# Kernel optimization log

Measured on AMD Instinct MI355X. Metric: run time of the kernel, lower is better.

The kernel has to match this reference:

```python
import jax, jax.numpy as jnp
import numpy as np

B, N, TF, DM = 16, 4096, 512, 1024

def next_fast_len(n):
    # smallest 5-smooth number >= n (matches scipy.fftpack.next_fast_len)
    while True:
        m = n
        for p in (2, 3, 5):
            while m % p == 0:
                m //= p
        if m == 1:
            return n
        n += 1

def conv1d_fft(x, weights):
    # x: (..., N, F), weights: (M,); causal exponentially-weighted correlation
    n = x.shape[-2]
    m = weights.shape[-1]
    L = next_fast_len(n + m - 1)
    f_x = jnp.fft.rfft(x, n=L, axis=-2)                 # (..., Lr, F) complex
    f_w = jnp.fft.rfft(weights, n=L, axis=-1)           # (Lr,)
    out = jnp.fft.irfft(f_x * jnp.conj(f_w)[..., None], L, axis=-2)
    out = jnp.roll(out, -1, axis=-2)
    return out[..., L - n:, :]                           # last N along seq axis

def setup_inputs() -> dict:
    key = jax.random.key(0)
    ks = jax.random.split(key, 8)
    inp = {
        "x": jax.random.normal(ks[0], (B, N, TF), dtype=jnp.float32),
        "latent_growth": jax.random.normal(ks[1], (B, N, DM), dtype=jnp.float32),
        "latent_seasonal": jax.random.normal(ks[2], (B, N, DM), dtype=jnp.float32),
        "alpha": jnp.zeros((1,), dtype=jnp.float32),  # nn.Parameter(torch.Tensor([0.0]))
        "w_growth": jax.random.normal(ks[3], (TF, DM), dtype=jnp.float32) / np.sqrt(DM),
        "b_growth": jnp.zeros((TF,), dtype=jnp.float32),
        "w_seasonal": jax.random.normal(ks[4], (TF, DM), dtype=jnp.float32) / np.sqrt(DM),
        "b_seasonal": jnp.zeros((TF,), dtype=jnp.float32),
    }
    return inp

def reference(x, latent_growth, latent_seasonal, alpha, w_growth, b_growth, w_seasonal, b_seasonal):
    n = x.shape[1]
    a = jax.nn.sigmoid(alpha)[0]
    powers = jnp.arange(n, dtype=x.dtype)[::-1]          # flipped arange
    seasonal = jnp.einsum('bnd,fd->bnf', latent_seasonal, w_seasonal) + b_seasonal
    aes_weights = a * (1.0 - a) ** powers                # alpha*(1-alpha)^k EMA kernel
    seasonal_normalized_term = conv1d_fft(x - seasonal, aes_weights)
    # NOTE: the original module computes `growth` but does not use it in the output
    growth = jnp.einsum('bnd,fd->bnf', latent_growth, w_growth) + b_growth
    growth_term = conv1d_fft(x, aes_weights)
    return seasonal_normalized_term + growth_term
```

## Files before the change

### kernel.cpp

```cpp
#include <hip/hip_runtime.h>
#include <math.h>

#define B_DIM 16
#define N_SEQ 4096
#define TF_DIM 512
#define DM_DIM 1024
#define CHUNK 128
#define NCHUNK (N_SEQ / CHUNK)
#define NKT (DM_DIM / 32)

typedef __attribute__((ext_vector_type(4))) float f32x4;
typedef __attribute__((ext_vector_type(8))) short bf16x8;
typedef unsigned short u16;
typedef unsigned int u32;

__device__ __forceinline__ u16 f2bf(float f) {
    u32 u = __builtin_bit_cast(u32, f);
    u += 0x7fffu + ((u >> 16) & 1u);
    return (u16)(u >> 16);
}

__device__ __forceinline__ u32 cvtpk(float lo, float hi) {
    u32 r;
    asm("v_cvt_pk_bf16_f32 %0, %1, %2" : "=v"(r) : "v"(lo), "v"(hi));
    return r;
}

__device__ __forceinline__ void gload16(const u16* g, u16* l) {
    __builtin_amdgcn_global_load_lds(
        (const __attribute__((address_space(1))) void*)g,
        (__attribute__((address_space(3))) void*)l, 16, 0, 0);
}

#define SYNC_DRAIN() asm volatile("s_waitcnt vmcnt(0)\n\ts_barrier" ::: "memory")

__global__ __launch_bounds__(256)
void cvt_bf16(const float* __restrict__ ls, const float* __restrict__ wm,
              u16* __restrict__ lsb, u16* __restrict__ wmb)
{
    const size_t LSG = (size_t)B_DIM * N_SEQ * DM_DIM / 4;
    const size_t i = (size_t)blockIdx.x * 256 + threadIdx.x;
    const float* src;
    u16* dst;
    if (i < LSG) { src = ls + i * 4; dst = lsb + i * 4; }
    else         { const size_t j = i - LSG; src = wm + j * 4; dst = wmb + j * 4; }
    const f32x4 v = *(const f32x4*)src;
    u32* d = (u32*)dst;
    d[0] = cvtpk(v[0], v[1]);
    d[1] = cvtpk(v[2], v[3]);
}

__global__ __launch_bounds__(256, 2)
void gemm_u_kernel(const float* __restrict__ x,
                   const u16* __restrict__ lsb,
                   const u16* __restrict__ wmb,
                   const float* __restrict__ bias,
                   const float* __restrict__ alpha,
                   u16* __restrict__ u,
                   float* __restrict__ e)
{
    __shared__ u16 As[2][4096];
    __shared__ u16 Ws[2][4096];
    __shared__ float red[2][4][16];

    const int tid = threadIdx.x;

    const int s  = blockIdx.x;
    const int kk = s >> 3;
    const int fb = kk & 3;
    const int rp = (s & 7) + ((kk >> 2) << 3);
    const int f0   = fb * 128;
    const int row0 = rp * 128;

    const int lane = tid & 63;
    const int wid  = tid >> 6;
    const int wm = wid >> 1, wn = wid & 1;
    const int l15 = lane & 15, l4 = lane >> 4;

    const int G0 = wid * 128 + lane;
    const int G1 = G0 + 64;
    int row_a, slot_a, row_b, slot_b;
    { const int r = G0 >> 2;
      row_a  = (r & ~1) | ((r ^ (G0 >> 4)) & 1);
      slot_a = (G0 & 3) ^ (row_a & 3); }
    { const int r = G1 >> 2;
      row_b  = (r & ~1) | ((r ^ (G1 >> 4)) & 1);
      slot_b = (G1 & 3) ^ (row_b & 3); }

    const u16* aSrc0 = lsb + (size_t)(row0 + row_a) * DM_DIM + slot_a * 8;
    const u16* aSrc1 = lsb + (size_t)(row0 + row_b) * DM_DIM + slot_b * 8;
    const u16* wSrc0 = wmb + (size_t)(f0 + row_a) * DM_DIM + slot_a * 8;
    const u16* wSrc1 = wmb + (size_t)(f0 + row_b) * DM_DIM + slot_b * 8;

#define STAGE(BUF, KT) do {                                              \
        const int _o = (KT) * 32;                                        \
        gload16(aSrc0 + _o, &As[BUF][wid * 1024]);                       \
        gload16(aSrc1 + _o, &As[BUF][wid * 1024 + 512]);                 \
        gload16(wSrc0 + _o, &Ws[BUF][wid * 1024]);                       \
        gload16(wSrc1 + _o, &Ws[BUF][wid * 1024 + 512]);                 \
    } while (0)

    int rofa[4], rofw[4];
    const int rxor = (l15 & 7) << 3;
#pragma unroll
    for (int i = 0; i < 4; ++i) {
        rofa[i] = ((wm * 64 + i * 16 + l15) * 32 + l4 * 8) ^ rxor;
        rofw[i] = ((wn * 64 + i * 16 + l15) * 32 + l4 * 8) ^ rxor;
    }

    f32x4 acc[4][4];
#pragma unroll
    for (int i = 0; i < 4; ++i)
#pragma unroll
        for (int j = 0; j < 4; ++j) acc[i][j] = (f32x4){0.f, 0.f, 0.f, 0.f};

#define COMPUTE(BUF) do {                                                \
        const u16* _Ab = As[BUF];                                        \
        const u16* _Wb = Ws[BUF];                                        \
        bf16x8 _af[4], _wf[4];                                           \
        _Pragma("unroll")                                                \
        for (int i = 0; i < 4; ++i) {                                    \
            _af[i] = *(const bf16x8*)(_Ab + rofa[i]);                    \
            _wf[i] = *(const bf16x8*)(_Wb + rofw[i]);                    \
        }                                                                \
        _Pragma("unroll")                                                \
        for (int mi = 0; mi < 4; ++mi)                                   \
        _Pragma("unroll")                                                \
        for (int ni = 0; ni < 4; ++ni)                                   \
            acc[mi][ni] = __builtin_amdgcn_mfma_f32_16x16x32_bf16(       \
                _af[mi], _wf[ni], acc[mi][ni], 0, 0, 0);                 \
    } while (0)

    STAGE(0, 0);
    SYNC_DRAIN();

#pragma unroll 1
    for (int kt = 0; kt < NKT; kt += 2) {
        if (kt + 1 < NKT) STAGE(1, kt + 1);
        COMPUTE(0);
        SYNC_DRAIN();

        if (kt + 2 < NKT) STAGE(0, kt + 2);
        COMPUTE(1);
        SYNC_DRAIN();
    }

    const float a = 1.0f / (1.0f + expf(-alpha[0]));
    const float c = 1.0f - a;
    const float l2c = log2f(c);

    float bia[4];
#pragma unroll
    for (int ni = 0; ni < 4; ++ni) bia[ni] = bias[f0 + wn * 64 + ni * 16 + l15];

    float epart[4] = {0.f, 0.f, 0.f, 0.f};

#pragma unroll
    for (int mi = 0; mi < 4; ++mi) {
#pragma unroll
        for (int j = 0; j < 4; ++j) {
            const int r = wm * 64 + mi * 16 + l4 * 4 + j;
            const size_t rb = (size_t)(row0 + r) * TF_DIM;
            const float wgt = (r == CHUNK - 1)
                                  ? a
                                  : a * exp2f((float)(CHUNK - 1 - r) * l2c);
#pragma unroll
            for (int ni = 0; ni < 4; ++ni) {
                const int f = f0 + wn * 64 + ni * 16 + l15;
                const float uval = 2.0f * x[rb + f] - (acc[mi][ni][j] + bia[ni]);
                u[rb + f] = f2bf(uval);
                epart[ni] = fmaf(wgt, uval, epart[ni]);
            }
        }
    }

#pragma unroll
    for (int ni = 0; ni < 4; ++ni) {
        epart[ni] += __shfl_xor(epart[ni], 16, 64);
        epart[ni] += __shfl_xor(epart[ni], 32, 64);
    }
    if (wm == 1 && l4 == 0) {
#pragma unroll
        for (int ni = 0; ni < 4; ++ni) red[wn][ni][l15] = epart[ni];
    }
    __syncthreads();
    if (wm == 0 && l4 == 0) {
#pragma unroll
        for (int ni = 0; ni < 4; ++ni) {
            const int f = f0 + wn * 64 + ni * 16 + l15;
            e[(size_t)rp * TF_DIM + f] = epart[ni] + red[wn][ni][l15];
        }
    }
}

__global__ __launch_bounds__(256)
void ema_carry(const float* __restrict__ e, const float* __restrict__ alpha,
               float* __restrict__ carry)
{
    const int idx = blockIdx.x * 256 + threadIdx.x;
    const int f = idx & (TF_DIM - 1);
    const int b = idx >> 9;
    const float a = 1.0f / (1.0f + expf(-alpha[0]));
    const float c = 1.0f - a;
    const float cC = exp2f((float)CHUNK * log2f(c));
    const size_t base = (size_t)b * NCHUNK * TF_DIM + f;
    float Y = 0.0f;
    carry[base] = 0.0f;
    for (int ch = 1; ch < NCHUNK; ++ch) {
        Y = fmaf(cC, Y, e[base + (size_t)(ch - 1) * TF_DIM]);
        carry[base + (size_t)ch * TF_DIM] = Y;
    }
}

__global__ __launch_bounds__(256)
void ema_apply(const u16* __restrict__ u, const float* __restrict__ carry,
               const float* __restrict__ alpha, float* __restrict__ out)
{
    const int bc = blockIdx.x;
    const int tid = threadIdx.x;
    const float a = 1.0f / (1.0f + expf(-alpha[0]));
    const float c = 1.0f - a;
    float y0 = carry[(size_t)bc * TF_DIM + 2 * tid];
    float y1 = carry[(size_t)bc * TF_DIM + 2 * tid + 1];
    const u32* up = (const u32*)(u + (size_t)bc * CHUNK * TF_DIM) + tid;
    float2*    op = (float2*)(out + (size_t)bc * CHUNK * TF_DIM) + tid;
#pragma unroll 4
    for (int j = 0; j < CHUNK; ++j) {
        const u32 w = up[(size_t)j * (TF_DIM / 2)];
        const float u0 = __builtin_bit_cast(float, (w & 0xffffu) << 16);
        const float u1 = __builtin_bit_cast(float, (w >> 16) << 16);
        y0 = fmaf(c, y0, a * u0);
        y1 = fmaf(c, y1, a * u1);
        op[(size_t)j * (TF_DIM / 2)] = make_float2(y0, y1);
    }
}

extern "C" void kernel_launch(void* const* d_in, const int* in_sizes, int n_in,
                              void* d_out, int out_size, void* d_ws, size_t ws_size,
                              hipStream_t stream) {
    const float* x     = (const float*)d_in[0];
    const float* ls    = (const float*)d_in[2];
    const float* alpha = (const float*)d_in[3];
    const float* wmat  = (const float*)d_in[6];
    const float* bias  = (const float*)d_in[7];
    float* out = (float*)d_out;

    u16*   u     = (u16*)d_ws;
    u16*   lsb   = u + (size_t)B_DIM * N_SEQ * TF_DIM;
    u16*   wmb   = lsb + (size_t)B_DIM * N_SEQ * DM_DIM;
    float* e     = (float*)(wmb + (size_t)TF_DIM * DM_DIM);
    float* carry = e + (size_t)B_DIM * NCHUNK * TF_DIM;

    const int cvt_blocks = (B_DIM * N_SEQ * DM_DIM / 4 + TF_DIM * DM_DIM / 4) / 256;
    cvt_bf16<<<cvt_blocks, 256, 0, stream>>>(ls, wmat, lsb, wmb);

    gemm_u_kernel<<<2048, 256, 0, stream>>>(x, lsb, wmb, bias, alpha, u, e);

    ema_carry<<<(B_DIM * TF_DIM) / 256, 256, 0, stream>>>(e, alpha, carry);
    ema_apply<<<B_DIM * NCHUNK, 256, 0, stream>>>(u, carry, alpha, out);
}
```

Measured before the change: 253.3 us.

## Enlarge GEMM tile to 256x128 with 512-thread blocks and simpler LDS swizzle

After: 244.4 us. -3.5%, faster.

```diff
diff --git a/kernel.cpp b/kernel.cpp
--- a/kernel.cpp
+++ b/kernel.cpp
@@ -50,7 +50,7 @@
     d[1] = cvtpk(v[2], v[3]);
 }
 
-__global__ __launch_bounds__(256, 2)
+__global__ __launch_bounds__(512, 4)
 void gemm_u_kernel(const float* __restrict__ x,
                    const u16* __restrict__ lsb,
                    const u16* __restrict__ wmb,
@@ -59,9 +59,9 @@
                    u16* __restrict__ u,
                    float* __restrict__ e)
 {
-    __shared__ u16 As[2][4096];
+    __shared__ u16 As[2][8192];
     __shared__ u16 Ws[2][4096];
-    __shared__ float red[2][4][16];
+    __shared__ float red[2][2][4][16];
 
     const int tid = threadIdx.x;
 
@@ -70,42 +70,32 @@
     const int fb = kk & 3;
     const int rp = (s & 7) + ((kk >> 2) << 3);
     const int f0   = fb * 128;
-    const int row0 = rp * 128;
+    const int row0 = rp * 256;
 
     const int lane = tid & 63;
     const int wid  = tid >> 6;
     const int wm = wid >> 1, wn = wid & 1;
     const int l15 = lane & 15, l4 = lane >> 4;
 
-    const int G0 = wid * 128 + lane;
-    const int G1 = G0 + 64;
-    int row_a, slot_a, row_b, slot_b;
-    { const int r = G0 >> 2;
-      row_a  = (r & ~1) | ((r ^ (G0 >> 4)) & 1);
-      slot_a = (G0 & 3) ^ (row_a & 3); }
-    { const int r = G1 >> 2;
-      row_b  = (r & ~1) | ((r ^ (G1 >> 4)) & 1);
-      slot_b = (G1 & 3) ^ (row_b & 3); }
-
-    const u16* aSrc0 = lsb + (size_t)(row0 + row_a) * DM_DIM + slot_a * 8;
-    const u16* aSrc1 = lsb + (size_t)(row0 + row_b) * DM_DIM + slot_b * 8;
-    const u16* wSrc0 = wmb + (size_t)(f0 + row_a) * DM_DIM + slot_a * 8;
-    const u16* wSrc1 = wmb + (size_t)(f0 + row_b) * DM_DIM + slot_b * 8;
+    const int srow = lane >> 2;
+    const int sgc  = (lane & 3) ^ (srow & 3);
+    const u16* pA = lsb + (size_t)(row0 + wid * 32 + srow) * DM_DIM + sgc * 8;
+    const u16* pW = wmb + (size_t)(f0 + wid * 16 + srow) * DM_DIM + sgc * 8;
 
 #define STAGE(BUF, KT) do {                                              \
         const int _o = (KT) * 32;                                        \
-        gload16(aSrc0 + _o, &As[BUF][wid * 1024]);                       \
-        gload16(aSrc1 + _o, &As[BUF][wid * 1024 + 512]);                 \
-        gload16(wSrc0 + _o, &Ws[BUF][wid * 1024]);                       \
-        gload16(wSrc1 + _o, &Ws[BUF][wid * 1024 + 512]);                 \
+        gload16(pA + _o,                 &As[BUF][wid * 1024]);          \
+        gload16(pA + _o + 16 * DM_DIM,   &As[BUF][wid * 1024 + 512]);    \
+        gload16(pW + _o,                 &Ws[BUF][wid * 512]);           \
     } while (0)
 
     int rofa[4], rofw[4];
-    const int rxor = (l15 & 7) << 3;
 #pragma unroll
     for (int i = 0; i < 4; ++i) {
-        rofa[i] = ((wm * 64 + i * 16 + l15) * 32 + l4 * 8) ^ rxor;
-        rofw[i] = ((wn * 64 + i * 16 + l15) * 32 + l4 * 8) ^ rxor;
+        const int ra = wm * 64 + i * 16 + l15;
+        const int rw = wn * 64 + i * 16 + l15;
+        rofa[i] = ra * 32 + ((l4 ^ (ra & 3)) * 8);
+        rofw[i] = rw * 32 + ((l4 ^ (rw & 3)) * 8);
     }
 
     f32x4 acc[4][4];
@@ -160,10 +150,11 @@
 #pragma unroll
         for (int j = 0; j < 4; ++j) {
             const int r = wm * 64 + mi * 16 + l4 * 4 + j;
+            const int rc = r & (CHUNK - 1);
             const size_t rb = (size_t)(row0 + r) * TF_DIM;
-            const float wgt = (r == CHUNK - 1)
+            const float wgt = (rc == CHUNK - 1)
                                   ? a
-                                  : a * exp2f((float)(CHUNK - 1 - r) * l2c);
+                                  : a * exp2f((float)(CHUNK - 1 - rc) * l2c);
 #pragma unroll
             for (int ni = 0; ni < 4; ++ni) {
                 const int f = f0 + wn * 64 + ni * 16 + l15;
@@ -179,16 +170,17 @@
         epart[ni] += __shfl_xor(epart[ni], 16, 64);
         epart[ni] += __shfl_xor(epart[ni], 32, 64);
     }
-    if (wm == 1 && l4 == 0) {
-#pragma unroll
-        for (int ni = 0; ni < 4; ++ni) red[wn][ni][l15] = epart[ni];
+    const int ch = wm >> 1;
+    if ((wm & 1) == 1 && l4 == 0) {
+#pragma unroll
+        for (int ni = 0; ni < 4; ++ni) red[ch][wn][ni][l15] = epart[ni];
     }
     __syncthreads();
-    if (wm == 0 && l4 == 0) {
+    if ((wm & 1) == 0 && l4 == 0) {
 #pragma unroll
         for (int ni = 0; ni < 4; ++ni) {
             const int f = f0 + wn * 64 + ni * 16 + l15;
-            e[(size_t)rp * TF_DIM + f] = epart[ni] + red[wn][ni][l15];
+            e[(size_t)(rp * 2 + ch) * TF_DIM + f] = epart[ni] + red[ch][wn][ni][l15];
         }
     }
 }
@@ -254,7 +246,7 @@
     const int cvt_blocks = (B_DIM * N_SEQ * DM_DIM / 4 + TF_DIM * DM_DIM / 4) / 256;
     cvt_bf16<<<cvt_blocks, 256, 0, stream>>>(ls, wmat, lsb, wmb);
 
-    gemm_u_kernel<<<2048, 256, 0, stream>>>(x, lsb, wmb, bias, alpha, u, e);
+    gemm_u_kernel<<<1024, 512, 0, stream>>>(x, lsb, wmb, bias, alpha, u, e);
 
     ema_carry<<<(B_DIM * TF_DIM) / 256, 256, 0, stream>>>(e, alpha, carry);
     ema_apply<<<B_DIM * NCHUNK, 256, 0, stream>>>(u, carry, alpha, out);
```
